# Performance work log

Hardware: AMD Instinct MI355X
Metric: run time of the kernel (lower is better)

Reference implementation:

```python
import jax, jax.numpy as jnp
import numpy as np

HEADS = 8
DIM_HEAD = 64
QLEVEL = 127.0  # symmetric int8: clamp to [-128, 127]


def fake_quant(x):
    """Symmetric per-tensor int8 fake quantization with straight-through estimator."""
    delta = jnp.max(jnp.abs(x)) / QLEVEL
    xq = jnp.clip(jnp.round(x / delta), -128.0, 127.0) * delta
    return x + jax.lax.stop_gradient(xq - x)


def setup_inputs() -> dict:
    key = jax.random.key(0)
    ks = jax.random.split(key, 7)
    b, n, m, d, dc = 2, 4096, 1024, 512, 768
    return {
        "x": jax.random.normal(ks[0], (b, n, d), jnp.float32),
        "context": jax.random.normal(ks[1], (b, m, dc), jnp.float32),
        "Wq": jax.random.normal(ks[2], (d, d), jnp.float32) * 0.02,
        "Wk": jax.random.normal(ks[3], (dc, d), jnp.float32) * 0.02,
        "Wv": jax.random.normal(ks[4], (dc, d), jnp.float32) * 0.02,
        "Wo": jax.random.normal(ks[5], (d, d), jnp.float32) * 0.02,
        "bo": jnp.zeros((d,), jnp.float32),
    }


def reference(x, context, Wq, Wk, Wv, Wo, bo):
    b, n, _ = x.shape
    h, dh = HEADS, DIM_HEAD
    scale = dh ** -0.5

    q = x @ Wq            # [b, n, h*dh]
    k = context @ Wk      # [b, m, h*dh]
    v = context @ Wv      # [b, m, h*dh]

    def split(t):  # b n (h d) -> b h n d
        return t.reshape(t.shape[0], t.shape[1], h, dh).transpose(0, 2, 1, 3)

    q, k, v = split(q), split(k), split(v)

    # fake-quantize q and k before the score matmul (use_aq=True path)
    q = fake_quant(q)
    k = fake_quant(k)
    sim = jnp.einsum('bhid,bhjd->bhij', q, k) * scale  # [b, h, n, m]
    attn = jax.nn.softmax(sim, axis=-1)

    # fake-quantize attention weights and v before the AV matmul
    out = jnp.einsum('bhij,bhjd->bhid', fake_quant(attn), fake_quant(v))
    out = out.transpose(0, 2, 1, 3).reshape(b, n, h * dh)  # b h n d -> b n (h d)
    return out @ Wo + bo  # to_out[0]; to_out[-1] is Dropout (identity in eval)
```

## Files before the change

### kernel.cpp

```cpp
#include <hip/hip_runtime.h>
#include <stdint.h>

typedef float  v4f  __attribute__((ext_vector_type(4)));
typedef int    v4i  __attribute__((ext_vector_type(4)));
typedef __bf16 v8bf __attribute__((ext_vector_type(8)));
typedef __bf16 v4bf __attribute__((ext_vector_type(4)));

#define BATCH  2
#define NQ     4096
#define MK     1024
#define DMODEL 512
#define DCTX   768
#define NH     8
#define DH     64

__global__ __launch_bounds__(256) void k_prep(
    const float* __restrict__ Wq, const float* __restrict__ Wk,
    const float* __restrict__ Wv, const float* __restrict__ Wo,
    __bf16* __restrict__ Wq_t, __bf16* __restrict__ Wk_t,
    __bf16* __restrict__ Wv_t, __bf16* __restrict__ Wo_t,
    unsigned* __restrict__ scal) {
  int id = blockIdx.x;
  if (id == 0 && threadIdx.x < 4) scal[threadIdx.x] = 0u;
  int tx = id & 15, rem = id >> 4;
  int ty = rem % 24, tz = rem / 24;
  const float* src; __bf16* dst; int K;
  switch (tz) {
    case 0:  src = Wq; dst = Wq_t; K = DMODEL; break;
    case 1:  src = Wk; dst = Wk_t; K = DCTX;   break;
    case 2:  src = Wv; dst = Wv_t; K = DCTX;   break;
    default: src = Wo; dst = Wo_t; K = DMODEL; break;
  }
  int k0 = ty * 32;
  if (k0 >= K) return;
  int n0 = tx * 32;
  __shared__ __bf16 tile[32][33];
  int c = threadIdx.x & 31, r0 = threadIdx.x >> 5;
  for (int i = 0; i < 4; ++i) {
    int r = r0 + i * 8;
    tile[c][r] = (__bf16)src[(size_t)(k0 + r) * DMODEL + n0 + c];
  }
  __syncthreads();
  for (int i = 0; i < 4; ++i) {
    int r = r0 + i * 8;
    dst[(size_t)(n0 + r) * K + k0 + c] = tile[r][c];
  }
}

__device__ __forceinline__ v8bf load_a8(const __bf16* p) {
  return *(const v8bf*)p;
}
__device__ __forceinline__ v8bf load_a8(const float* p) {
  float4 a = *(const float4*)p, b = *(const float4*)(p + 4);
  v8bf o = { (__bf16)a.x, (__bf16)a.y, (__bf16)a.z, (__bf16)a.w,
             (__bf16)b.x, (__bf16)b.y, (__bf16)b.z, (__bf16)b.w };
  return o;
}

template<int K_, int NC, bool BIAS, bool AMAX, typename AT>
__device__ __forceinline__ void gemm_body(
    char* smemraw, const AT* __restrict__ A, const __bf16* __restrict__ Bt,
    float* __restrict__ C, int N, int rowBlk, int colBlk,
    const float* __restrict__ bias,
    unsigned* __restrict__ amaxLo, unsigned* __restrict__ amaxHi) {
  constexpr int CS = K_ + 8;
  constexpr int GPC = K_ / 8;
  constexpr int JT = NC / 16;
  __bf16* Bs = (__bf16*)smemraw;
  float* redmax = (float*)(smemraw + (size_t)NC * CS * 2);
  const int tid = threadIdx.x;
  const int lane = tid & 63, wave = tid >> 6;
  const int l15 = lane & 15, g = lane >> 4;
  const int col0 = colBlk * NC;
  const int row0w = rowBlk * 128 + wave * 32;

#pragma unroll
  for (int i = 0; i < NC * GPC / 256; ++i) {
    int f = i * 256 + tid;
    int c = f / GPC, w = f - c * GPC;
    *(v8bf*)(&Bs[c * CS + w * 8]) =
        *(const v8bf*)(Bt + (size_t)(col0 + c) * K_ + w * 8);
  }
  __syncthreads();

  v4f acc[2][JT] = {};
  const AT* a0 = A + (size_t)(row0w + l15) * K_ + g * 8;
  const AT* a1 = A + (size_t)(row0w + 16 + l15) * K_ + g * 8;
#pragma unroll
  for (int k0 = 0; k0 < K_; k0 += 32) {
    v8bf af0 = load_a8(a0 + k0);
    v8bf af1 = load_a8(a1 + k0);
#pragma unroll
    for (int j = 0; j < JT; ++j) {
      v8bf bfj = *(const v8bf*)(&Bs[(j * 16 + l15) * CS + k0 + g * 8]);
      acc[0][j] = __builtin_amdgcn_mfma_f32_16x16x32_bf16(af0, bfj, acc[0][j], 0, 0, 0);
      acc[1][j] = __builtin_amdgcn_mfma_f32_16x16x32_bf16(af1, bfj, acc[1][j], 0, 0, 0);
    }
  }

  float lmax = 0.0f;
#pragma unroll
  for (int j = 0; j < JT; ++j) {
    int col = col0 + j * 16 + l15;
    float bv = BIAS ? bias[col] : 0.0f;
#pragma unroll
    for (int i = 0; i < 2; ++i) {
#pragma unroll
      for (int r = 0; r < 4; ++r) {
        int row = row0w + i * 16 + g * 4 + r;
        float cv = acc[i][j][r] + bv;
        C[(size_t)row * N + col] = cv;
        if (AMAX) lmax = fmaxf(lmax, fabsf(cv));
      }
    }
  }
  if (AMAX) {
    for (int off = 32; off > 0; off >>= 1)
      lmax = fmaxf(lmax, __shfl_xor(lmax, off, 64));
    if (lane == 0) redmax[wave] = lmax;
    __syncthreads();
    if (tid == 0) {
      float bm = fmaxf(fmaxf(redmax[0], redmax[1]), fmaxf(redmax[2], redmax[3]));
      atomicMax(col0 < 512 ? amaxLo : amaxHi, __float_as_uint(bm));
    }
  }
}

__global__ __launch_bounds__(256, 2) void k_gemm_qkv(
    const float* __restrict__ x, const __bf16* __restrict__ Wq_t,
    float* __restrict__ qf,
    const float* __restrict__ ctx, const __bf16* __restrict__ Wkv_t,
    float* __restrict__ kvf, unsigned* __restrict__ scal) {
  __shared__ __align__(16) char smem[64 * (512 + 8) * 2 + 16];
  int bid = blockIdx.x;
  if (bid < 512) {
    int xcd = bid & 7, w = bid >> 3;
    gemm_body<512, 64, false, true, float>(smem, x, Wq_t, qf, 512,
                                           xcd * 8 + (w >> 3), w & 7, nullptr,
                                           scal + 0, scal + 0);
  } else {
    int id = bid - 512;
    int xcd = id & 7, w = id >> 3;
    gemm_body<768, 32, false, true, float>(smem, ctx, Wkv_t, kvf, 1024,
                                           xcd * 2 + (w >> 5), w & 31, nullptr,
                                           scal + 1, scal + 2);
  }
}

__global__ __launch_bounds__(256, 2) void k_gemm_out(
    const __bf16* __restrict__ o, const __bf16* __restrict__ Wo_t,
    float* __restrict__ out, const float* __restrict__ bo) {
  __shared__ __align__(16) char smem[64 * (512 + 8) * 2 + 16];
  int xcd = blockIdx.x & 7, w = blockIdx.x >> 3;
  gemm_body<512, 64, true, false, __bf16>(smem, o, Wo_t, out, 512,
                                          xcd * 8 + (w >> 3), w & 7, bo,
                                          nullptr, nullptr);
}

__global__ __launch_bounds__(256) void k_quant_kv(
    const float* __restrict__ kvf,
    int8_t* __restrict__ k8, int8_t* __restrict__ v8t,
    const unsigned* __restrict__ scal) {
  __shared__ int8_t tile[64][80];
  int bx = blockIdx.x;
  if (bx < 1024) {
    int j = bx * 256 + threadIdx.x;
    int r = j >> 7;
    int c4 = (j & 127) << 2;
    float4 v = *(const float4*)(kvf + (size_t)r * 1024 + c4);
    float s = 127.0f / __uint_as_float(scal[1]);
    int a0 = __float2int_rn(v.x * s), a1 = __float2int_rn(v.y * s);
    int a2 = __float2int_rn(v.z * s), a3 = __float2int_rn(v.w * s);
    a0 = max(-128, min(127, a0)); a1 = max(-128, min(127, a1));
    a2 = max(-128, min(127, a2)); a3 = max(-128, min(127, a3));
    unsigned p = (unsigned)(a0 & 255) | ((unsigned)(a1 & 255) << 8) |
                 ((unsigned)(a2 & 255) << 16) | ((unsigned)(a3 & 255) << 24);
    *(unsigned*)(k8 + (size_t)j * 4) = p;
    return;
  }
  int id = bx - 1024;
  int bh = id >> 4, b = bh >> 3, h = bh & 7;
  int j0 = (id & 15) * 64;
  const float s = 127.0f / __uint_as_float(scal[2]);
  int t = threadIdx.x;
  int j = t >> 2, dh0 = (t & 3) << 4;
  const float* src = kvf + (size_t)(b * MK + j0 + j) * 1024 + 512 + h * DH + dh0;
#pragma unroll
  for (int i = 0; i < 16; i += 4) {
    float4 v = *(const float4*)(src + i);
    int a0 = __float2int_rn(v.x * s), a1 = __float2int_rn(v.y * s);
    int a2 = __float2int_rn(v.z * s), a3 = __float2int_rn(v.w * s);
    tile[dh0 + i + 0][j] = (int8_t)max(-128, min(127, a0));
    tile[dh0 + i + 1][j] = (int8_t)max(-128, min(127, a1));
    tile[dh0 + i + 2][j] = (int8_t)max(-128, min(127, a2));
    tile[dh0 + i + 3][j] = (int8_t)max(-128, min(127, a3));
  }
  __syncthreads();
  int dh = t >> 2, jb = (t & 3) << 4;
  v4i val = *(const v4i*)(&tile[dh][jb]);
  *(v4i*)(v8t + (size_t)(bh * DH + dh) * MK + j0 + jb) = val;
}

__device__ __forceinline__ v4i quant_pack16(const float* p, float s) {
  v4i out;
#pragma unroll
  for (int q = 0; q < 4; ++q) {
    float4 v = *(const float4*)(p + q * 4);
    int a0 = __float2int_rn(v.x * s), a1 = __float2int_rn(v.y * s);
    int a2 = __float2int_rn(v.z * s), a3 = __float2int_rn(v.w * s);
    a0 = max(-128, min(127, a0)); a1 = max(-128, min(127, a1));
    a2 = max(-128, min(127, a2)); a3 = max(-128, min(127, a3));
    out[q] = (int)((unsigned)(a0 & 255) | ((unsigned)(a1 & 255) << 8) |
                   ((unsigned)(a2 & 255) << 16) | ((unsigned)(a3 & 255) << 24));
  }
  return out;
}

__global__ __launch_bounds__(256, 4) void k_pass1(
    const float* __restrict__ qf, int8_t* __restrict__ q8,
    const int8_t* __restrict__ k8,
    float* __restrict__ invz, unsigned* __restrict__ scal) {
  __shared__ __align__(16) int8_t kbuf[128 * 72];
  __shared__ float mared[4];
  int bh = blockIdx.y, b = bh >> 3, h = bh & 7;
  int wave = threadIdx.x >> 6, lane = threadIdx.x & 63;
  int l15 = lane & 15, g = lane >> 4;
  int row0 = blockIdx.x * 64;
  int myrow = row0 + wave * 16 + l15;
  const float aq = __uint_as_float(scal[0]), ak = __uint_as_float(scal[1]);
  const float alpha2 = (aq * ak) * (0.125f / (127.0f * 127.0f)) * 1.44269504f;
  const float sq = 127.0f / aq;
  const v4i z4 = {0, 0, 0, 0};
  size_t qoff = (size_t)(b * NQ + myrow) * DMODEL + h * DH + g * 16;
  v4i qfrag = quant_pack16(qf + qoff, sq);
  *(v4i*)(q8 + qoff) = qfrag;
  const int8_t* kbase = k8 + (size_t)b * MK * DMODEL + h * DH;
  const int rs = threadIdx.x >> 2, qs = (threadIdx.x & 3) * 16;
  const int8_t* kls = kbase + (size_t)rs * DMODEL + qs;

  v4i kp0 = *(const v4i*)(kls);
  v4i kp1 = *(const v4i*)(kls + (size_t)64 * DMODEL);

  float z[4] = {0.f, 0.f, 0.f, 0.f};
  int mi = -(1 << 30);
  for (int tile = 0; tile < 8; ++tile) {
    __syncthreads();
    *(v4i*)(&kbuf[rs * 72 + qs]) = kp0;
    *(v4i*)(&kbuf[(rs + 64) * 72 + qs]) = kp1;
    __syncthreads();
    if (tile < 7) {
      kp0 = *(const v4i*)(kls + (size_t)((tile + 1) * 128) * DMODEL);
      kp1 = *(const v4i*)(kls + (size_t)((tile + 1) * 128 + 64) * DMODEL);
    }
    float zt = z[tile >> 1];
#pragma unroll
    for (int t = 0; t < 8; ++t) {
      v4i kfrag = *(const v4i*)(&kbuf[(t * 16 + l15) * 72 + g * 16]);
      v4i sa = __builtin_amdgcn_mfma_i32_16x16x64_i8(kfrag, qfrag, z4, 0, 0, 0);
      mi = max(mi, max(max(sa[0], sa[1]), max(sa[2], sa[3])));
      float e0 = __builtin_amdgcn_exp2f((float)sa[0] * alpha2);
      float e1 = __builtin_amdgcn_exp2f((float)sa[1] * alpha2);
      float e2 = __builtin_amdgcn_exp2f((float)sa[2] * alpha2);
      float e3 = __builtin_amdgcn_exp2f((float)sa[3] * alpha2);
      zt += (e0 + e1) + (e2 + e3);
    }
    z[tile >> 1] = zt;
  }
#pragma unroll
  for (int i = 0; i < 4; ++i) {
    z[i] += __shfl_xor(z[i], 16, 64);
    z[i] += __shfl_xor(z[i], 32, 64);
  }
  mi = max(mi, __shfl_xor(mi, 16, 64));
  mi = max(mi, __shfl_xor(mi, 32, 64));
  float zt = (z[0] + z[1]) + (z[2] + z[3]);
  float iz = 1.0f / zt;
  if (g == 0) invz[(size_t)bh * NQ + myrow] = iz;
  float ma = __builtin_amdgcn_exp2f((float)mi * alpha2) * iz;
#pragma unroll
  for (int off = 1; off < 16; off <<= 1)
    ma = fmaxf(ma, __shfl_xor(ma, off, 64));
  if (lane == 0) mared[wave] = ma;
  __syncthreads();
  if (threadIdx.x == 0)
    atomicMax(scal + 3,
              __float_as_uint(fmaxf(fmaxf(mared[0], mared[1]),
                                    fmaxf(mared[2], mared[3]))));
}

__global__ __launch_bounds__(256, 4) void k_pass2(
    const int8_t* __restrict__ q8, const int8_t* __restrict__ k8,
    const int8_t* __restrict__ v8t, const float* __restrict__ invz,
    const unsigned* __restrict__ scal, __bf16* __restrict__ o) {
  __shared__ __align__(16) int8_t kbuf[128 * 72];
  __shared__ __align__(16) int8_t vbuf[64 * 152];
  __shared__ __align__(16) int8_t albuf[4][16 * 152];
  int bh = blockIdx.y, b = bh >> 3, h = bh & 7;
  int wave = threadIdx.x >> 6, lane = threadIdx.x & 63;
  int l15 = lane & 15, g = lane >> 4;
  int row0 = blockIdx.x * 64;
  int myrow = row0 + wave * 16 + l15;
  const float aq = __uint_as_float(scal[0]), ak = __uint_as_float(scal[1]);
  const float avv = __uint_as_float(scal[2]), izm = __uint_as_float(scal[3]);
  const float alpha2 = (aq * ak) * (0.125f / (127.0f * 127.0f)) * 1.44269504f;
  const float oscale = (izm / 127.0f) * (avv / 127.0f);
  const float MAGIC = 12582912.0f;
  const v4i z4 = {0, 0, 0, 0};

  v4i qfrag = *(const v4i*)(q8 + (size_t)(b * NQ + myrow) * DMODEL + h * DH + g * 16);
  const float lcr = __builtin_amdgcn_logf(invz[(size_t)bh * NQ + myrow] * (127.0f / izm));
  const int8_t* kbase = k8 + (size_t)b * MK * DMODEL + h * DH;
  const int8_t* vbase = v8t + (size_t)bh * DH * MK;
  int8_t* alds = albuf[wave];
  const int rs = threadIdx.x >> 2, qs = (threadIdx.x & 3) * 16;
  const int vr = threadIdx.x >> 3, vq = (threadIdx.x & 7) * 16;
  const int8_t* kls = kbase + (size_t)rs * DMODEL + qs;
  const int8_t* vls = vbase + (size_t)vr * MK + vq;

  v4i kp0 = *(const v4i*)(kls);
  v4i kp1 = *(const v4i*)(kls + (size_t)64 * DMODEL);
  v4i vp0 = *(const v4i*)(vls);
  v4i vp1 = *(const v4i*)(vls + (size_t)32 * MK);

  v4i pacc[4] = {};
  for (int tile = 0; tile < 8; ++tile) {
    __syncthreads();
    *(v4i*)(&kbuf[rs * 72 + qs]) = kp0;
    *(v4i*)(&kbuf[(rs + 64) * 72 + qs]) = kp1;
    *(v4i*)(&vbuf[vr * 152 + vq]) = vp0;
    *(v4i*)(&vbuf[(vr + 32) * 152 + vq]) = vp1;
    __syncthreads();
    if (tile < 7) {
      kp0 = *(const v4i*)(kls + (size_t)((tile + 1) * 128) * DMODEL);
      kp1 = *(const v4i*)(kls + (size_t)((tile + 1) * 128 + 64) * DMODEL);
      vp0 = *(const v4i*)(vls + (tile + 1) * 128);
      vp1 = *(const v4i*)(vls + (size_t)32 * MK + (tile + 1) * 128);
    }
#pragma unroll
    for (int t = 0; t < 8; ++t) {
      v4i kfrag = *(const v4i*)(&kbuf[(t * 16 + l15) * 72 + g * 16]);
      v4i sa = __builtin_amdgcn_mfma_i32_16x16x64_i8(kfrag, qfrag, z4, 0, 0, 0);
      float f0 = __builtin_amdgcn_exp2f(fmaf((float)sa[0], alpha2, lcr)) + MAGIC;
      float f1 = __builtin_amdgcn_exp2f(fmaf((float)sa[1], alpha2, lcr)) + MAGIC;
      float f2 = __builtin_amdgcn_exp2f(fmaf((float)sa[2], alpha2, lcr)) + MAGIC;
      float f3 = __builtin_amdgcn_exp2f(fmaf((float)sa[3], alpha2, lcr)) + MAGIC;
      unsigned packed = (__float_as_uint(f0) & 255u) |
                        ((__float_as_uint(f1) & 255u) << 8) |
                        ((__float_as_uint(f2) & 255u) << 16) |
                        (__float_as_uint(f3) << 24);
      *(unsigned*)(alds + l15 * 152 + t * 16 + g * 4) = packed;
    }
#pragma unroll
    for (int c = 0; c < 2; ++c) {
      v4i afrag = *(const v4i*)(alds + l15 * 152 + c * 64 + g * 16);
#pragma unroll
      for (int d = 0; d < 4; ++d) {
        v4i vfrag = *(const v4i*)(&vbuf[(d * 16 + l15) * 152 + c * 64 + g * 16]);
        pacc[d] = __builtin_amdgcn_mfma_i32_16x16x64_i8(vfrag, afrag, pacc[d], 0, 0, 0);
      }
    }
  }
  __bf16* obase = o + (size_t)(b * NQ + row0 + wave * 16 + l15) * DMODEL + h * DH;
#pragma unroll
  for (int d = 0; d < 4; ++d) {
    v4bf ov;
#pragma unroll
    for (int r = 0; r < 4; ++r)
      ov[r] = (__bf16)((float)pacc[d][r] * oscale);
    *(v4bf*)(obase + d * 16 + g * 4) = ov;
  }
}

extern "C" void kernel_launch(void* const* d_in, const int* in_sizes, int n_in,
                              void* d_out, int out_size, void* d_ws, size_t ws_size,
                              hipStream_t stream) {
  (void)in_sizes; (void)n_in; (void)out_size; (void)ws_size;
  const float* x   = (const float*)d_in[0];
  const float* ctx = (const float*)d_in[1];
  const float* Wq  = (const float*)d_in[2];
  const float* Wk  = (const float*)d_in[3];
  const float* Wv  = (const float*)d_in[4];
  const float* Wo  = (const float*)d_in[5];
  const float* bo  = (const float*)d_in[6];
  float* out = (float*)d_out;

  char* ws = (char*)d_ws;
  size_t off = 0;
  auto alloc = [&](size_t bytes) {
    char* p = ws + off;
    off += (bytes + 255) & ~(size_t)255;
    return p;
  };
  unsigned* scal = (unsigned*)alloc(16);
  __bf16* Wq_t = (__bf16*)alloc((size_t)512 * 512 * 2);
  __bf16* Wk_t = (__bf16*)alloc((size_t)512 * 768 * 2);
  __bf16* Wv_t = (__bf16*)alloc((size_t)512 * 768 * 2);
  __bf16* Wo_t = (__bf16*)alloc((size_t)512 * 512 * 2);
  float* qf  = (float*)alloc((size_t)BATCH * NQ * DMODEL * 4);
  float* kvf = (float*)alloc((size_t)BATCH * MK * 1024 * 4);
  int8_t* q8 = (int8_t*)alloc((size_t)BATCH * NQ * DMODEL);
  int8_t* k8 = (int8_t*)alloc((size_t)BATCH * MK * DMODEL);
  int8_t* v8t = (int8_t*)alloc((size_t)BATCH * NH * DH * MK);
  float* invz = (float*)alloc((size_t)BATCH * NH * NQ * 4);
  __bf16* o = (__bf16*)qf;

  k_prep<<<1536, 256, 0, stream>>>(Wq, Wk, Wv, Wo,
                                   Wq_t, Wk_t, Wv_t, Wo_t, scal);
  k_gemm_qkv<<<1024, 256, 0, stream>>>(x, Wq_t, qf, ctx, Wk_t, kvf, scal);
  k_quant_kv<<<1280, 256, 0, stream>>>(kvf, k8, v8t, scal);
  k_pass1<<<dim3(64, 16), 256, 0, stream>>>(qf, q8, k8, invz, scal);
  k_pass2<<<dim3(64, 16), 256, 0, stream>>>(q8, k8, v8t, invz, scal, o);
  k_gemm_out<<<512, 256, 0, stream>>>(o, Wo_t, out, bo);
}
```

Before: 193.5 us.

## Pre-convert GEMM inputs to bf16 and software-pipeline A and B fragment loads

Adds a bulk fp32-to-bf16 conversion of x and context into the prep kernel, so the QKV GEMM reads bf16 directly. The GEMM inner loop now prefetches A fragments from global memory four k-steps ahead and double-buffers B fragments from shared memory, overlapping loads with MFMA issue. The cost is an extra pass writing and re-reading bf16 copies of the activations, and more registers held per thread, which could affect occupancy.

```diff
diff --git a/kernel.cpp b/kernel.cpp
--- a/kernel.cpp
+++ b/kernel.cpp
@@ -15,12 +15,32 @@
 #define DH     64
 
 __global__ __launch_bounds__(256) void k_prep(
+    const float* __restrict__ x, const float* __restrict__ ctx,
+    __bf16* __restrict__ xb, __bf16* __restrict__ cb,
     const float* __restrict__ Wq, const float* __restrict__ Wk,
     const float* __restrict__ Wv, const float* __restrict__ Wo,
     __bf16* __restrict__ Wq_t, __bf16* __restrict__ Wk_t,
     __bf16* __restrict__ Wv_t, __bf16* __restrict__ Wo_t,
     unsigned* __restrict__ scal) {
-  int id = blockIdx.x;
+  int bx = blockIdx.x;
+  if (bx < 2816) {
+    const int XC = BATCH * NQ * DMODEL / 8;
+    const int CC = BATCH * MK * DCTX / 8;
+    int idx = bx * 256 + threadIdx.x;
+    const float* src; __bf16* dst;
+    if (idx < XC) { src = x + (size_t)idx * 8; dst = xb + (size_t)idx * 8; }
+    else {
+      int j = idx - XC;
+      if (j >= CC) return;
+      src = ctx + (size_t)j * 8; dst = cb + (size_t)j * 8;
+    }
+    float4 a = *(const float4*)src, b = *(const float4*)(src + 4);
+    v8bf o = { (__bf16)a.x, (__bf16)a.y, (__bf16)a.z, (__bf16)a.w,
+               (__bf16)b.x, (__bf16)b.y, (__bf16)b.z, (__bf16)b.w };
+    *(v8bf*)dst = o;
+    return;
+  }
+  int id = bx - 2816;
   if (id == 0 && threadIdx.x < 4) scal[threadIdx.x] = 0u;
   int tx = id & 15, rem = id >> 4;
   int ty = rem % 24, tz = rem / 24;
@@ -47,25 +67,17 @@
   }
 }
 
-__device__ __forceinline__ v8bf load_a8(const __bf16* p) {
-  return *(const v8bf*)p;
-}
-__device__ __forceinline__ v8bf load_a8(const float* p) {
-  float4 a = *(const float4*)p, b = *(const float4*)(p + 4);
-  v8bf o = { (__bf16)a.x, (__bf16)a.y, (__bf16)a.z, (__bf16)a.w,
-             (__bf16)b.x, (__bf16)b.y, (__bf16)b.z, (__bf16)b.w };
-  return o;
-}
-
-template<int K_, int NC, bool BIAS, bool AMAX, typename AT>
+template<int K_, int NC, bool BIAS, bool AMAX>
 __device__ __forceinline__ void gemm_body(
-    char* smemraw, const AT* __restrict__ A, const __bf16* __restrict__ Bt,
+    char* smemraw, const __bf16* __restrict__ A, const __bf16* __restrict__ Bt,
     float* __restrict__ C, int N, int rowBlk, int colBlk,
     const float* __restrict__ bias,
     unsigned* __restrict__ amaxLo, unsigned* __restrict__ amaxHi) {
   constexpr int CS = K_ + 8;
   constexpr int GPC = K_ / 8;
   constexpr int JT = NC / 16;
+  constexpr int NIT = K_ / 32;
+  constexpr int AD = 4;
   __bf16* Bs = (__bf16*)smemraw;
   float* redmax = (float*)(smemraw + (size_t)NC * CS * 2);
   const int tid = threadIdx.x;
@@ -81,20 +93,43 @@
     *(v8bf*)(&Bs[c * CS + w * 8]) =
         *(const v8bf*)(Bt + (size_t)(col0 + c) * K_ + w * 8);
   }
+
+  const __bf16* a0 = A + (size_t)(row0w + l15) * K_ + g * 8;
+  const __bf16* a1 = A + (size_t)(row0w + 16 + l15) * K_ + g * 8;
+
+  v8bf abuf0[AD], abuf1[AD];
+#pragma unroll
+  for (int i = 0; i < AD; ++i) {
+    abuf0[i] = *(const v8bf*)(a0 + i * 32);
+    abuf1[i] = *(const v8bf*)(a1 + i * 32);
+  }
   __syncthreads();
 
+  v8bf bbuf[2][JT];
+#pragma unroll
+  for (int j = 0; j < JT; ++j)
+    bbuf[0][j] = *(const v8bf*)(&Bs[(j * 16 + l15) * CS + g * 8]);
+
   v4f acc[2][JT] = {};
-  const AT* a0 = A + (size_t)(row0w + l15) * K_ + g * 8;
-  const AT* a1 = A + (size_t)(row0w + 16 + l15) * K_ + g * 8;
-#pragma unroll
-  for (int k0 = 0; k0 < K_; k0 += 32) {
-    v8bf af0 = load_a8(a0 + k0);
-    v8bf af1 = load_a8(a1 + k0);
+#pragma unroll
+  for (int it = 0; it < NIT; ++it) {
+    const int cur = it & 1, nxt = cur ^ 1;
+    if (it + 1 < NIT) {
+#pragma unroll
+      for (int j = 0; j < JT; ++j)
+        bbuf[nxt][j] =
+            *(const v8bf*)(&Bs[(j * 16 + l15) * CS + (it + 1) * 32 + g * 8]);
+    }
+    v8bf af0 = abuf0[it % AD];
+    v8bf af1 = abuf1[it % AD];
+    if (it + AD < NIT) {
+      abuf0[it % AD] = *(const v8bf*)(a0 + (it + AD) * 32);
+      abuf1[it % AD] = *(const v8bf*)(a1 + (it + AD) * 32);
+    }
 #pragma unroll
     for (int j = 0; j < JT; ++j) {
-      v8bf bfj = *(const v8bf*)(&Bs[(j * 16 + l15) * CS + k0 + g * 8]);
-      acc[0][j] = __builtin_amdgcn_mfma_f32_16x16x32_bf16(af0, bfj, acc[0][j], 0, 0, 0);
-      acc[1][j] = __builtin_amdgcn_mfma_f32_16x16x32_bf16(af1, bfj, acc[1][j], 0, 0, 0);
+      acc[0][j] = __builtin_amdgcn_mfma_f32_16x16x32_bf16(af0, bbuf[cur][j], acc[0][j], 0, 0, 0);
+      acc[1][j] = __builtin_amdgcn_mfma_f32_16x16x32_bf16(af1, bbuf[cur][j], acc[1][j], 0, 0, 0);
     }
   }
 
@@ -127,23 +162,23 @@
 }
 
 __global__ __launch_bounds__(256, 2) void k_gemm_qkv(
-    const float* __restrict__ x, const __bf16* __restrict__ Wq_t,
+    const __bf16* __restrict__ xb, const __bf16* __restrict__ Wq_t,
     float* __restrict__ qf,
-    const float* __restrict__ ctx, const __bf16* __restrict__ Wkv_t,
+    const __bf16* __restrict__ cb, const __bf16* __restrict__ Wkv_t,
     float* __restrict__ kvf, unsigned* __restrict__ scal) {
   __shared__ __align__(16) char smem[64 * (512 + 8) * 2 + 16];
   int bid = blockIdx.x;
   if (bid < 512) {
     int xcd = bid & 7, w = bid >> 3;
-    gemm_body<512, 64, false, true, float>(smem, x, Wq_t, qf, 512,
-                                           xcd * 8 + (w >> 3), w & 7, nullptr,
-                                           scal + 0, scal + 0);
+    gemm_body<512, 64, false, true>(smem, xb, Wq_t, qf, 512,
+                                    xcd * 8 + (w >> 3), w & 7, nullptr,
+                                    scal + 0, scal + 0);
   } else {
     int id = bid - 512;
     int xcd = id & 7, w = id >> 3;
-    gemm_body<768, 32, false, true, float>(smem, ctx, Wkv_t, kvf, 1024,
-                                           xcd * 2 + (w >> 5), w & 31, nullptr,
-                                           scal + 1, scal + 2);
+    gemm_body<768, 32, false, true>(smem, cb, Wkv_t, kvf, 1024,
+                                    xcd * 2 + (w >> 5), w & 31, nullptr,
+                                    scal + 1, scal + 2);
   }
 }
 
@@ -152,9 +187,9 @@
     float* __restrict__ out, const float* __restrict__ bo) {
   __shared__ __align__(16) char smem[64 * (512 + 8) * 2 + 16];
   int xcd = blockIdx.x & 7, w = blockIdx.x >> 3;
-  gemm_body<512, 64, true, false, __bf16>(smem, o, Wo_t, out, 512,
-                                          xcd * 8 + (w >> 3), w & 7, bo,
-                                          nullptr, nullptr);
+  gemm_body<512, 64, true, false>(smem, o, Wo_t, out, 512,
+                                  xcd * 8 + (w >> 3), w & 7, bo,
+                                  nullptr, nullptr);
 }
 
 __global__ __launch_bounds__(256) void k_quant_kv(
@@ -396,6 +431,8 @@
   __bf16* Wk_t = (__bf16*)alloc((size_t)512 * 768 * 2);
   __bf16* Wv_t = (__bf16*)alloc((size_t)512 * 768 * 2);
   __bf16* Wo_t = (__bf16*)alloc((size_t)512 * 512 * 2);
+  __bf16* xb   = (__bf16*)alloc((size_t)BATCH * NQ * DMODEL * 2);
+  __bf16* cb   = (__bf16*)alloc((size_t)BATCH * MK * DCTX * 2);
   float* qf  = (float*)alloc((size_t)BATCH * NQ * DMODEL * 4);
   float* kvf = (float*)alloc((size_t)BATCH * MK * 1024 * 4);
   int8_t* q8 = (int8_t*)alloc((size_t)BATCH * NQ * DMODEL);
@@ -404,9 +441,9 @@
   float* invz = (float*)alloc((size_t)BATCH * NH * NQ * 4);
   __bf16* o = (__bf16*)qf;
 
-  k_prep<<<1536, 256, 0, stream>>>(Wq, Wk, Wv, Wo,
+  k_prep<<<4352, 256, 0, stream>>>(x, ctx, xb, cb, Wq, Wk, Wv, Wo,
                                    Wq_t, Wk_t, Wv_t, Wo_t, scal);
-  k_gemm_qkv<<<1024, 256, 0, stream>>>(x, Wq_t, qf, ctx, Wk_t, kvf, scal);
+  k_gemm_qkv<<<1024, 256, 0, stream>>>(xb, Wq_t, qf, cb, Wk_t, kvf, scal);
   k_quant_kv<<<1280, 256, 0, stream>>>(kvf, k8, v8t, scal);
   k_pass1<<<dim3(64, 16), 256, 0, stream>>>(qf, q8, k8, invz, scal);
   k_pass2<<<dim3(64, 16), 256, 0, stream>>>(q8, k8, v8t, invz, scal, o);
```

New measurement: 178.0 us. 1.09x faster.
